# Performance work log

Measured on AMD Instinct MI355X. Metric: run time of the kernel, lower is better.

## Reference

```python
import jax, jax.numpy as jnp
import numpy as np

B, T, E, H, C = 64, 512, 768, 128, 18


def setup_inputs() -> dict:
    key = jax.random.key(0)
    ks = jax.random.split(key, 16)
    s = 1.0 / np.sqrt(H)
    inp = {
        "x": jax.random.normal(ks[0], (B, T, E), jnp.float32),
        "attention_mask": jnp.ones((B, T), jnp.int32),
        "labels": jax.random.randint(ks[1], (B, T), 0, C, jnp.int32),
        "Wih_f": jax.random.uniform(ks[2], (4 * H, E), jnp.float32, -s, s),
        "Whh_f": jax.random.uniform(ks[3], (4 * H, H), jnp.float32, -s, s),
        "b_f": jax.random.uniform(ks[4], (4 * H,), jnp.float32, -s, s),
        "Wih_b": jax.random.uniform(ks[5], (4 * H, E), jnp.float32, -s, s),
        "Whh_b": jax.random.uniform(ks[6], (4 * H, H), jnp.float32, -s, s),
        "b_b": jax.random.uniform(ks[7], (4 * H,), jnp.float32, -s, s),
        "Wfc": jax.random.uniform(ks[8], (C, 2 * H), jnp.float32, -s, s),
        "bfc": jax.random.uniform(ks[9], (C,), jnp.float32, -s, s),
        "start_trans": jax.random.normal(ks[10], (C,), jnp.float32) * 0.1,
        "end_trans": jax.random.normal(ks[11], (C,), jnp.float32) * 0.1,
        "trans": jax.random.normal(ks[12], (C, C), jnp.float32) * 0.1,
    }
    return inp


def _lstm_dir(x, Wih, Whh, b, reverse=False):
    # x: [B, T, E] -> hidden states [B, T, H]; torch LSTM gate order i,f,g,o
    if reverse:
        x = x[:, ::-1]
    pre = jnp.einsum("bte,ge->btg", x, Wih) + b  # [B, T, 4H] input projection once
    h0 = jnp.zeros((x.shape[0], H), x.dtype)

    def step(carry, pt):
        h, c = carry
        g = pt + h @ Whh.T
        i, f, gg, o = jnp.split(g, 4, axis=-1)
        c = jax.nn.sigmoid(f) * c + jax.nn.sigmoid(i) * jnp.tanh(gg)
        h = jax.nn.sigmoid(o) * jnp.tanh(c)
        return (h, c), h

    _, hs = jax.lax.scan(step, (h0, h0), jnp.swapaxes(pre, 0, 1))
    hs = jnp.swapaxes(hs, 0, 1)
    if reverse:
        hs = hs[:, ::-1]
    return hs


def _crf_loglik(em, tags, mask, start, end, trans):
    # pytorch-crf log-likelihood, batch_first. em [B,T,C], tags/mask [B,T]
    b, t, _ = em.shape
    maskf = mask.astype(em.dtype)
    tags = tags.astype(jnp.int32)
    # numerator: score of the given tag path
    em_sc = jnp.take_along_axis(em, tags[..., None], axis=2)[..., 0]  # [B,T]
    num = start[tags[:, 0]] + em_sc[:, 0]
    num = num + jnp.sum(em_sc[:, 1:] * maskf[:, 1:], axis=1)
    num = num + jnp.sum(trans[tags[:, :-1], tags[:, 1:]] * maskf[:, 1:], axis=1)
    last_idx = jnp.sum(mask.astype(jnp.int32), axis=1) - 1
    last_tags = jnp.take_along_axis(tags, last_idx[:, None], axis=1)[:, 0]
    num = num + end[last_tags]
    # denominator: forward algorithm (logsumexp recurrence over time)
    alpha0 = start + em[:, 0]  # [B,C]

    def step(alpha, inp):
        e_t, m_t = inp
        new = jax.scipy.special.logsumexp(alpha[:, :, None] + trans[None], axis=1) + e_t
        return jnp.where(m_t[:, None], new, alpha), None

    alpha, _ = jax.lax.scan(
        step, alpha0,
        (jnp.swapaxes(em[:, 1:], 0, 1), jnp.swapaxes(mask[:, 1:].astype(bool), 0, 1)),
    )
    den = jax.scipy.special.logsumexp(alpha + end, axis=1)
    return num - den


def _viterbi(em, start, end, trans):
    # em [B,T,C] -> best path [B,T] (full mask)
    s0 = start + em[:, 0]

    def fstep(score, e_t):
        cand = score[:, :, None] + trans[None]  # [B,C,C]
        return jnp.max(cand, axis=1) + e_t, jnp.argmax(cand, axis=1)

    score, bptr = jax.lax.scan(fstep, s0, jnp.swapaxes(em[:, 1:], 0, 1))  # bptr [T-1,B,C]
    last = jnp.argmax(score + end, axis=1)  # [B]

    def bstep(tag, ptr_t):
        prev = jnp.take_along_axis(ptr_t, tag[:, None], axis=1)[:, 0]
        return prev, prev

    _, path = jax.lax.scan(bstep, last, bptr, reverse=True)  # [T-1,B]
    return jnp.concatenate([jnp.swapaxes(path, 0, 1), last[:, None]], axis=1)


def reference(x, attention_mask, labels, Wih_f, Whh_f, b_f, Wih_b, Whh_b, b_b,
              Wfc, bfc, start_trans, end_trans, trans):
    hf = _lstm_dir(x, Wih_f, Whh_f, b_f, reverse=False)
    hb = _lstm_dir(x, Wih_b, Whh_b, b_b, reverse=True)
    seq = jnp.concatenate([hf, hb], axis=-1)  # [B,T,2H]
    em = seq @ Wfc.T + bfc  # [B,T,C] emissions
    mask = attention_mask.astype(bool)
    llh = _crf_loglik(em, labels, mask, start_trans, end_trans, trans)
    loss = -jnp.sum(llh) / x.shape[0]  # reduction='sum' then / batch_size
    path = _viterbi(em, start_trans, end_trans, trans) + 1  # res_paths = x+1
    return path, loss
```

## Files before the change

### kernel.cpp

```cpp
#include <hip/hip_runtime.h>
#include <hip/hip_bf16.h>
#include <math.h>

typedef __attribute__((ext_vector_type(8))) short short8;
typedef __attribute__((ext_vector_type(4))) float f32x4;

constexpr int nB = 64, nT = 512, nE = 768, nH = 128, nG = 512, nC = 18;
constexpr int nBT = nB * nT;

__device__ __forceinline__ float bf2f(unsigned short u) { return __uint_as_float(((unsigned int)u) << 16); }
__device__ __forceinline__ unsigned short f2bf(float f) {
  __hip_bfloat16 h = __float2bfloat16(f);
  return *reinterpret_cast<unsigned short*>(&h);
}
__device__ __forceinline__ float fast_sig(float x) {
  return __builtin_amdgcn_rcpf(1.0f + __builtin_amdgcn_exp2f(-1.44269504f * x));
}
__device__ __forceinline__ float fast_tanh(float x) {
  return 1.0f - 2.0f * __builtin_amdgcn_rcpf(1.0f + __builtin_amdgcn_exp2f(2.88539008f * x));
}
__device__ __forceinline__ float fast_exp(float x) { return __builtin_amdgcn_exp2f(1.44269504f * x); }
__device__ __forceinline__ float fast_log(float x) { return __builtin_amdgcn_logf(x) * 0.69314718f; }

__global__ __launch_bounds__(256) void cvt_kernel(const float* __restrict__ in,
                                                  unsigned short* __restrict__ out, int n8) {
  int i = blockIdx.x * blockDim.x + threadIdx.x;
  const int stride = gridDim.x * blockDim.x;
  for (; i < n8; i += stride) {
    const float4 a = ((const float4*)in)[(size_t)i * 2];
    const float4 b = ((const float4*)in)[(size_t)i * 2 + 1];
    unsigned short u[8] = {f2bf(a.x), f2bf(a.y), f2bf(a.z), f2bf(a.w),
                           f2bf(b.x), f2bf(b.y), f2bf(b.z), f2bf(b.w)};
    ((float4*)out)[i] = *(float4*)u;
  }
}

__global__ __launch_bounds__(256) void proj_kernel(
    const unsigned short* __restrict__ xbf,
    const unsigned short* __restrict__ wfb, const unsigned short* __restrict__ wbb,
    const float* __restrict__ biasF, const float* __restrict__ biasB,
    unsigned short* __restrict__ Pf, unsigned short* __restrict__ Pb)
{
  const int bid = blockIdx.x;
  const int mt = bid & 255, sub = bid >> 8;
  const int dir = sub >> 2, nt = sub & 3;
  const unsigned short* W = dir ? wbb : wfb;
  const float* bias = dir ? biasB : biasF;
  unsigned short* P = dir ? Pb : Pf;
  const int m0 = mt * 128, n0 = nt * 128;

  __shared__ unsigned short As[128 * 40];
  __shared__ unsigned short Bs[128 * 40];
  const int tid = threadIdx.x;
  const int w = tid >> 6, lane = tid & 63, l15 = lane & 15, l4 = lane >> 4;
  const int wr = w >> 1, wc = w & 1;
  const int srow = tid >> 1, shalf = tid & 1;

  const unsigned short* srcA = xbf + (size_t)(m0 + srow) * nE + shalf * 16;
  const unsigned short* srcB = W + (size_t)(n0 + srow) * nE + shalf * 16;

  f32x4 acc[4][4];
#pragma unroll
  for (int i = 0; i < 4; ++i)
#pragma unroll
    for (int j = 0; j < 4; ++j) acc[i][j] = (f32x4){0.f, 0.f, 0.f, 0.f};

  for (int k0 = 0; k0 < nE; k0 += 32) {
    const float4 a0 = *(const float4*)(srcA + k0);
    const float4 a1 = *(const float4*)(srcA + k0 + 8);
    const float4 b0 = *(const float4*)(srcB + k0);
    const float4 b1 = *(const float4*)(srcB + k0 + 8);
    __syncthreads();
    *(float4*)&As[srow * 40 + shalf * 16] = a0;
    *(float4*)&As[srow * 40 + shalf * 16 + 8] = a1;
    *(float4*)&Bs[srow * 40 + shalf * 16] = b0;
    *(float4*)&Bs[srow * 40 + shalf * 16 + 8] = b1;
    __syncthreads();
    short8 af[4], bfr[4];
#pragma unroll
    for (int i = 0; i < 4; ++i) af[i] = *(const short8*)&As[(wr * 64 + i * 16 + l15) * 40 + l4 * 8];
#pragma unroll
    for (int j = 0; j < 4; ++j) bfr[j] = *(const short8*)&Bs[(wc * 64 + j * 16 + l15) * 40 + l4 * 8];
#pragma unroll
    for (int i = 0; i < 4; ++i)
#pragma unroll
      for (int j = 0; j < 4; ++j)
        acc[i][j] = __builtin_amdgcn_mfma_f32_16x16x32_bf16(af[i], bfr[j], acc[i][j], 0, 0, 0);
  }
  float bv[4];
#pragma unroll
  for (int j = 0; j < 4; ++j) bv[j] = bias[n0 + wc * 64 + j * 16 + l15];
#pragma unroll
  for (int i = 0; i < 4; ++i) {
#pragma unroll
    for (int j = 0; j < 4; ++j) {
      const int col = n0 + wc * 64 + j * 16 + l15;
#pragma unroll
      for (int r = 0; r < 4; ++r) {
        const int row = m0 + wr * 64 + i * 16 + l4 * 4 + r;
        P[(size_t)row * nG + col] = f2bf(acc[i][j][r] + bv[j]);
      }
    }
  }
}

__global__ __launch_bounds__(512, 1) void lstm_kernel(
    const unsigned short* __restrict__ Pf, const unsigned short* __restrict__ Pb,
    const float* __restrict__ WhhF, const float* __restrict__ WhhB,
    unsigned short* __restrict__ hf, unsigned short* __restrict__ hb)
{
  const int bid = blockIdx.x;
  const int dir = bid & 1, grp = bid >> 1;
  const int b0 = grp * 4;
  const unsigned short* pre = dir ? Pb : Pf;
  const float* Whh = dir ? WhhB : WhhF;
  unsigned short* hout = dir ? hb : hf;

  const int tid = threadIdx.x, w = tid >> 6, lane = tid & 63;
  const int l15 = lane & 15, l4 = lane >> 4;
  const int batch = l15 & 3, msel = l15 >> 2;
  const int cell = w * 16 + msel * 4 + l4;
  const int swz = batch * 40;

  __shared__ unsigned short h_lds[2 * 4 * 128];

  short8 Af[4][4];
#pragma unroll
  for (int m = 0; m < 4; ++m) {
    const int gp = w * 64 + m * 16 + l15;
    const int gorig = (gp & 3) * 128 + (gp >> 2);
#pragma unroll
    for (int kk = 0; kk < 4; ++kk) {
      const float* wp = Whh + (size_t)gorig * nH + kk * 32 + l4 * 8;
      const float4 v0 = *(const float4*)wp;
      const float4 v1 = *(const float4*)(wp + 4);
      unsigned short u[8] = {f2bf(v0.x), f2bf(v0.y), f2bf(v0.z), f2bf(v0.w),
                             f2bf(v1.x), f2bf(v1.y), f2bf(v1.z), f2bf(v1.w)};
      Af[m][kk] = *(short8*)u;
    }
  }
  for (int i = tid; i < 2 * 4 * 128; i += 512) h_lds[i] = 0;

  float c_state = 0.f;
  const unsigned short* pbase = pre + (size_t)(b0 + batch) * nT * nG + cell;

  unsigned short pA[4], pB[4];
  {
    const int tt0 = dir ? (nT - 1) : 0;
    const int tt1 = dir ? (nT - 2) : 1;
#pragma unroll
    for (int r = 0; r < 4; ++r) pA[r] = pbase[(size_t)tt0 * nG + r * 128];
#pragma unroll
    for (int r = 0; r < 4; ++r) pB[r] = pbase[(size_t)tt1 * nG + r * 128];
  }
  __syncthreads();

#define LSTM_STEP(RB, T, BUFC)                                                   \
  {                                                                              \
    const int ttime = dir ? (nT - 1 - (T)) : (T);                                \
    float pg[4];                                                                 \
    _Pragma("unroll")                                                            \
    for (int r = 0; r < 4; ++r) pg[r] = bf2f(BUFC[r]);                           \
    {                                                                            \
      const int tl = ((T) + 2 < nT) ? (T) + 2 : (T);                             \
      const int ttl = dir ? (nT - 1 - tl) : tl;                                  \
      _Pragma("unroll")                                                          \
      for (int r = 0; r < 4; ++r) BUFC[r] = pbase[(size_t)ttl * nG + r * 128];   \
    }                                                                            \
    short8 bfr[4];                                                               \
    _Pragma("unroll")                                                            \
    for (int kk = 0; kk < 4; ++kk) {                                             \
      const int idx = (RB) * 512 + batch * 128 + ((kk * 32 + l4 * 8) ^ swz);     \
      bfr[kk] = *(const short8*)&h_lds[idx];                                     \
    }                                                                            \
    f32x4 acc[4];                                                                \
    _Pragma("unroll")                                                            \
    for (int m = 0; m < 4; ++m) acc[m] = (f32x4){0.f, 0.f, 0.f, 0.f};            \
    _Pragma("unroll")                                                            \
    for (int kk = 0; kk < 4; ++kk)                                               \
      _Pragma("unroll")                                                          \
      for (int m = 0; m < 4; ++m)                                                \
        acc[m] = __builtin_amdgcn_mfma_f32_16x16x32_bf16(Af[m][kk], bfr[kk], acc[m], 0, 0, 0); \
    const float g0 = msel < 2 ? (msel == 0 ? acc[0][0] : acc[1][0]) : (msel == 2 ? acc[2][0] : acc[3][0]); \
    const float g1 = msel < 2 ? (msel == 0 ? acc[0][1] : acc[1][1]) : (msel == 2 ? acc[2][1] : acc[3][1]); \
    const float g2 = msel < 2 ? (msel == 0 ? acc[0][2] : acc[1][2]) : (msel == 2 ? acc[2][2] : acc[3][2]); \
    const float g3 = msel < 2 ? (msel == 0 ? acc[0][3] : acc[1][3]) : (msel == 2 ? acc[2][3] : acc[3][3]); \
    const float gi = g0 + pg[0], gf = g1 + pg[1], gg = g2 + pg[2], go = g3 + pg[3]; \
    c_state = fast_sig(gf) * c_state + fast_sig(gi) * fast_tanh(gg);             \
    const float hval = fast_sig(go) * fast_tanh(c_state);                        \
    const unsigned short hu = f2bf(hval);                                        \
    h_lds[((RB) ^ 1) * 512 + batch * 128 + (cell ^ swz)] = hu;                   \
    hout[((size_t)(b0 + batch) * nT + ttime) * nH + cell] = hu;                  \
    asm volatile("s_waitcnt lgkmcnt(0)" ::: "memory");                           \
    __builtin_amdgcn_sched_barrier(0);                                           \
    __builtin_amdgcn_s_barrier();                                                \
  }

  for (int t2 = 0; t2 < nT; t2 += 2) {
    LSTM_STEP(0, t2, pA)
    LSTM_STEP(1, t2 + 1, pB)
  }
#undef LSTM_STEP
}

__global__ __launch_bounds__(256) void em_kernel(
    const unsigned short* __restrict__ hf, const unsigned short* __restrict__ hb,
    const float* __restrict__ Wfc, const float* __restrict__ bfc,
    float* __restrict__ em)
{
  __shared__ float seq[32][260];
  __shared__ float Wf[18][260];
  const int tid = threadIdx.x;
  const int row0 = blockIdx.x * 32;
  for (int i = tid; i < 32 * 32; i += 256) {
    const int r = i >> 5, seg = i & 31;
    const unsigned short* src = (seg < 16) ? (hf + (size_t)(row0 + r) * nH + seg * 8)
                                           : (hb + (size_t)(row0 + r) * nH + (seg - 16) * 8);
    const float4 v = *(const float4*)src;
    const unsigned short* u = (const unsigned short*)&v;
#pragma unroll
    for (int k = 0; k < 8; ++k) seq[r][seg * 8 + k] = bf2f(u[k]);
  }
  for (int i = tid; i < nC * 256; i += 256) {
    const int cc = i >> 8, k = i & 255;
    Wf[cc][k] = Wfc[cc * 256 + k];
  }
  __syncthreads();
  for (int o = tid; o < 32 * nC; o += 256) {
    const int r = o / nC, cc = o - r * nC;
    float acc = bfc[cc];
    const float4* s4 = (const float4*)&seq[r][0];
    const float4* w4 = (const float4*)&Wf[cc][0];
#pragma unroll
    for (int q = 0; q < 64; ++q) {
      const float4 a = s4[q]; const float4 wv = w4[q];
      acc += a.x * wv.x + a.y * wv.y + a.z * wv.z + a.w * wv.w;
    }
    em[(size_t)(row0 + r) * nC + cc] = acc;
  }
}

__global__ __launch_bounds__(128) void crfvit_kernel(
    const float* __restrict__ em, const int* __restrict__ labels,
    const int* __restrict__ mask, const float* __restrict__ start,
    const float* __restrict__ endt, const float* __restrict__ trans,
    float* __restrict__ llh, float* __restrict__ out_path)
{
  const int b = blockIdx.x; const int tid = threadIdx.x;
  __shared__ float tr[nC * nC];
  __shared__ float alpha[nC];
  __shared__ float score[nC];
  __shared__ unsigned char bp[(nT - 1) * nC];
  __shared__ unsigned char path[nT];
  for (int i = tid; i < nC * nC; i += 128) tr[i] = trans[i];
  __syncthreads();
  const float* eb = em + (size_t)b * nT * nC;

  if (tid < 64) {
    const int l = tid;
    const int* tg = labels + (size_t)b * nT;
    const int* mk = mask + (size_t)b * nT;
    float np = 0.f; int cnt = 0;
    for (int t = l; t < nT; t += 64) {
      const int tag = tg[t];
      const float e = eb[(size_t)t * nC + tag];
      if (t == 0) np += start[tag] + e;
      else np += (float)mk[t] * (e + tr[tg[t - 1] * nC + tag]);
      cnt += mk[t];
    }
#pragma unroll
    for (int off = 32; off; off >>= 1) { np += __shfl_xor(np, off); cnt += __shfl_xor(cnt, off); }
    float num = np + endt[tg[cnt - 1]];

    if (l < nC) alpha[l] = start[l] + eb[l];
    float epre = (l < nC) ? eb[nC + l] : 0.f;
    __builtin_amdgcn_wave_barrier();
    for (int t = 1; t < nT; ++t) {
      const float ecur = epre;
      if (l < nC && t + 1 < nT) epre = eb[(size_t)(t + 1) * nC + l];
      float anew = 0.f;
      if (l < nC) {
        const float aold = alpha[l];
        float cand[nC];
        float m = -3.0e38f;
#pragma unroll
        for (int i = 0; i < nC; ++i) { cand[i] = alpha[i] + tr[i * nC + l]; m = fmaxf(m, cand[i]); }
        float s = 0.f;
#pragma unroll
        for (int i = 0; i < nC; ++i) s += fast_exp(cand[i] - m);
        anew = m + fast_log(s) + ecur;
        if (mk[t] == 0) anew = aold;
      }
      __builtin_amdgcn_wave_barrier();
      if (l < nC) alpha[l] = anew;
      __builtin_amdgcn_wave_barrier();
    }
    const float v = (l < nC) ? (alpha[l] + endt[l]) : -3.0e38f;
    float m = v;
#pragma unroll
    for (int off = 32; off; off >>= 1) m = fmaxf(m, __shfl_xor(m, off));
    float s = (l < nC) ? fast_exp(v - m) : 0.f;
#pragma unroll
    for (int off = 32; off; off >>= 1) s += __shfl_xor(s, off);
    if (l == 0) llh[b] = num - (m + fast_log(s));
  } else {
    const int l = tid - 64;
    if (l < nC) score[l] = start[l] + eb[l];
    float epre = (l < nC) ? eb[nC + l] : 0.f;
    __builtin_amdgcn_wave_barrier();
    for (int t = 1; t < nT; ++t) {
      const float ecur = epre;
      if (l < nC && t + 1 < nT) epre = eb[(size_t)(t + 1) * nC + l];
      float m = -3.0e38f; int arg = 0;
      if (l < nC) {
#pragma unroll
        for (int i = 0; i < nC; ++i) {
          const float v = score[i] + tr[i * nC + l];
          if (v > m) { m = v; arg = i; }
        }
        m += ecur;
      }
      __builtin_amdgcn_wave_barrier();
      if (l < nC) { score[l] = m; bp[(t - 1) * nC + l] = (unsigned char)arg; }
      __builtin_amdgcn_wave_barrier();
    }
    if (l == 0) {
      float m = -3.0e38f; int last = 0;
      for (int i = 0; i < nC; ++i) { const float v = score[i] + endt[i]; if (v > m) { m = v; last = i; } }
      path[nT - 1] = (unsigned char)last;
      int cur = last;
      for (int t = nT - 2; t >= 0; --t) { cur = bp[t * nC + cur]; path[t] = (unsigned char)cur; }
    }
    __builtin_amdgcn_wave_barrier();
    __builtin_amdgcn_s_waitcnt(0);
    for (int t = l; t < nT; t += 64) out_path[(size_t)b * nT + t] = (float)(path[t] + 1);
  }
}

__global__ __launch_bounds__(64) void loss_kernel(const float* __restrict__ llh, float* __restrict__ out)
{
  const int l = threadIdx.x;
  float v = llh[l];
#pragma unroll
  for (int off = 32; off; off >>= 1) v += __shfl_xor(v, off);
  if (l == 0) out[0] = -v / (float)nB;
}

extern "C" void kernel_launch(void* const* d_in, const int* in_sizes, int n_in,
                              void* d_out, int out_size, void* d_ws, size_t ws_size,
                              hipStream_t stream)
{
  const float* x      = (const float*)d_in[0];
  const int*   amask  = (const int*)d_in[1];
  const int*   labels = (const int*)d_in[2];
  const float* Wih_f  = (const float*)d_in[3];
  const float* Whh_f  = (const float*)d_in[4];
  const float* b_f    = (const float*)d_in[5];
  const float* Wih_b  = (const float*)d_in[6];
  const float* Whh_b  = (const float*)d_in[7];
  const float* b_b    = (const float*)d_in[8];
  const float* Wfc    = (const float*)d_in[9];
  const float* bfc    = (const float*)d_in[10];
  const float* start  = (const float*)d_in[11];
  const float* endt   = (const float*)d_in[12];
  const float* trans  = (const float*)d_in[13];

  float* out = (float*)d_out;
  float* ws = (float*)d_ws;
  unsigned short* preF = (unsigned short*)ws;
  unsigned short* preB = preF + (size_t)nBT * nG;
  unsigned short* hf   = preB + (size_t)nBT * nG;
  unsigned short* hb   = hf + (size_t)nBT * nH;
  float* em  = (float*)(hb + (size_t)nBT * nH);
  float* llh = em + (size_t)nBT * nC;
  unsigned short* xbf = (unsigned short*)(llh + 64);
  unsigned short* wfb = xbf + (size_t)nBT * nE;
  unsigned short* wbb = wfb + (size_t)nG * nE;

  cvt_kernel<<<4096, 256, 0, stream>>>(x, xbf, nBT * nE / 8);
  cvt_kernel<<<192, 256, 0, stream>>>(Wih_f, wfb, nG * nE / 8);
  cvt_kernel<<<192, 256, 0, stream>>>(Wih_b, wbb, nG * nE / 8);
  proj_kernel<<<2048, 256, 0, stream>>>(xbf, wfb, wbb, b_f, b_b, preF, preB);
  lstm_kernel<<<32, 512, 0, stream>>>(preF, preB, Whh_f, Whh_b, hf, hb);
  em_kernel<<<1024, 256, 0, stream>>>(hf, hb, Wfc, bfc, em);
  crfvit_kernel<<<64, 128, 0, stream>>>(em, labels, amask, start, endt, trans, llh, out);
  loss_kernel<<<1, 64, 0, stream>>>(llh, out + nBT);
}
```

Baseline: 630.0 us.

## Fuse x bf16 conversion into projection GEMM; register-resident CRF/Viterbi recurrences

Drops the separate kernel that converts x to bf16. The projection GEMM now loads fp32 x directly and converts it while staging into shared memory, which removes a full write and re-read of the bf16 copy of x. The CRF forward and Viterbi loops now keep alpha and score in registers and broadcast them with readlane instead of shared memory, using a register-cached transition column, a tree max, mask ballots, and a three-step emission prefetch. In exchange, the GEMM reads twice as many bytes per A tile and repeats the conversion in each N-tile block (8x redundant), and the CRF loops use more registers.

```diff
diff --git a/kernel.cpp b/kernel.cpp
--- a/kernel.cpp
+++ b/kernel.cpp
@@ -12,6 +12,9 @@
 __device__ __forceinline__ unsigned short f2bf(float f) {
   __hip_bfloat16 h = __float2bfloat16(f);
   return *reinterpret_cast<unsigned short*>(&h);
+}
+__device__ __forceinline__ float rlane(float v, int lane) {
+  return __uint_as_float(__builtin_amdgcn_readlane(__float_as_uint(v), lane));
 }
 __device__ __forceinline__ float fast_sig(float x) {
   return __builtin_amdgcn_rcpf(1.0f + __builtin_amdgcn_exp2f(-1.44269504f * x));
@@ -36,7 +39,7 @@
 }
 
 __global__ __launch_bounds__(256) void proj_kernel(
-    const unsigned short* __restrict__ xbf,
+    const float* __restrict__ x,
     const unsigned short* __restrict__ wfb, const unsigned short* __restrict__ wbb,
     const float* __restrict__ biasF, const float* __restrict__ biasB,
     unsigned short* __restrict__ Pf, unsigned short* __restrict__ Pb)
@@ -56,7 +59,7 @@
   const int wr = w >> 1, wc = w & 1;
   const int srow = tid >> 1, shalf = tid & 1;
 
-  const unsigned short* srcA = xbf + (size_t)(m0 + srow) * nE + shalf * 16;
+  const float* srcA = x + (size_t)(m0 + srow) * nE + shalf * 16;
   const unsigned short* srcB = W + (size_t)(n0 + srow) * nE + shalf * 16;
 
   f32x4 acc[4][4];
@@ -67,12 +70,18 @@
 
   for (int k0 = 0; k0 < nE; k0 += 32) {
     const float4 a0 = *(const float4*)(srcA + k0);
-    const float4 a1 = *(const float4*)(srcA + k0 + 8);
+    const float4 a1 = *(const float4*)(srcA + k0 + 4);
+    const float4 a2 = *(const float4*)(srcA + k0 + 8);
+    const float4 a3 = *(const float4*)(srcA + k0 + 12);
     const float4 b0 = *(const float4*)(srcB + k0);
     const float4 b1 = *(const float4*)(srcB + k0 + 8);
+    unsigned short ua[16] = {f2bf(a0.x), f2bf(a0.y), f2bf(a0.z), f2bf(a0.w),
+                             f2bf(a1.x), f2bf(a1.y), f2bf(a1.z), f2bf(a1.w),
+                             f2bf(a2.x), f2bf(a2.y), f2bf(a2.z), f2bf(a2.w),
+                             f2bf(a3.x), f2bf(a3.y), f2bf(a3.z), f2bf(a3.w)};
     __syncthreads();
-    *(float4*)&As[srow * 40 + shalf * 16] = a0;
-    *(float4*)&As[srow * 40 + shalf * 16 + 8] = a1;
+    *(float4*)&As[srow * 40 + shalf * 16] = *(float4*)&ua[0];
+    *(float4*)&As[srow * 40 + shalf * 16 + 8] = *(float4*)&ua[8];
     *(float4*)&Bs[srow * 40 + shalf * 16] = b0;
     *(float4*)&Bs[srow * 40 + shalf * 16 + 8] = b1;
     __syncthreads();
@@ -248,18 +257,22 @@
 {
   const int b = blockIdx.x; const int tid = threadIdx.x;
   __shared__ float tr[nC * nC];
-  __shared__ float alpha[nC];
-  __shared__ float score[nC];
   __shared__ unsigned char bp[(nT - 1) * nC];
   __shared__ unsigned char path[nT];
   for (int i = tid; i < nC * nC; i += 128) tr[i] = trans[i];
   __syncthreads();
   const float* eb = em + (size_t)b * nT * nC;
 
+#define MAX18(c) fmaxf(fmaxf(fmaxf(fmaxf(fmaxf(c[0], c[1]), c[2]), fmaxf(fmaxf(c[3], c[4]), c[5])),           \
+                             fmaxf(fmaxf(fmaxf(c[6], c[7]), c[8]), fmaxf(fmaxf(c[9], c[10]), c[11]))),        \
+                       fmaxf(fmaxf(fmaxf(c[12], c[13]), c[14]), fmaxf(fmaxf(c[15], c[16]), c[17])))
+
   if (tid < 64) {
     const int l = tid;
+    const int lc = l < nC ? l : nC - 1;
     const int* tg = labels + (size_t)b * nT;
     const int* mk = mask + (size_t)b * nT;
+
     float np = 0.f; int cnt = 0;
     for (int t = l; t < nT; t += 64) {
       const int tag = tg[t];
@@ -270,32 +283,38 @@
     }
 #pragma unroll
     for (int off = 32; off; off >>= 1) { np += __shfl_xor(np, off); cnt += __shfl_xor(cnt, off); }
-    float num = np + endt[tg[cnt - 1]];
-
-    if (l < nC) alpha[l] = start[l] + eb[l];
-    float epre = (l < nC) ? eb[nC + l] : 0.f;
-    __builtin_amdgcn_wave_barrier();
-    for (int t = 1; t < nT; ++t) {
-      const float ecur = epre;
-      if (l < nC && t + 1 < nT) epre = eb[(size_t)(t + 1) * nC + l];
-      float anew = 0.f;
-      if (l < nC) {
-        const float aold = alpha[l];
+    const float num = np + endt[tg[cnt - 1]];
+
+    float trc[nC];
+#pragma unroll
+    for (int i = 0; i < nC; ++i) trc[i] = tr[i * nC + lc];
+
+    float alpha_r = start[lc] + eb[lc];
+    float eA = eb[1 * nC + lc];
+    float eB = eb[2 * nC + lc];
+    float eC = eb[3 * nC + lc];
+    for (int tk = 0; tk < 8; ++tk) {
+      const unsigned long long mb = __ballot(mk[tk * 64 + l] != 0);
+      for (int tt = (tk == 0 ? 1 : 0); tt < 64; ++tt) {
+        const int t = tk * 64 + tt;
+        const float ecur = eA; eA = eB; eB = eC;
+        const int tl = t + 3 < nT ? t + 3 : nT - 1;
+        eC = eb[(size_t)tl * nC + lc];
         float cand[nC];
-        float m = -3.0e38f;
-#pragma unroll
-        for (int i = 0; i < nC; ++i) { cand[i] = alpha[i] + tr[i * nC + l]; m = fmaxf(m, cand[i]); }
+#pragma unroll
+        for (int i = 0; i < nC; ++i) cand[i] = rlane(alpha_r, i) + trc[i];
+        const float m = MAX18(cand);
+        float ex[nC];
+#pragma unroll
+        for (int i = 0; i < nC; ++i) ex[i] = fast_exp(cand[i] - m);
         float s = 0.f;
 #pragma unroll
-        for (int i = 0; i < nC; ++i) s += fast_exp(cand[i] - m);
-        anew = m + fast_log(s) + ecur;
-        if (mk[t] == 0) anew = aold;
+        for (int i = 0; i < nC; ++i) s += ex[i];
+        const float anew = m + fast_log(s) + ecur;
+        alpha_r = ((mb >> tt) & 1) ? anew : alpha_r;
       }
-      __builtin_amdgcn_wave_barrier();
-      if (l < nC) alpha[l] = anew;
-      __builtin_amdgcn_wave_barrier();
-    }
-    const float v = (l < nC) ? (alpha[l] + endt[l]) : -3.0e38f;
+    }
+    const float v = (l < nC) ? (alpha_r + endt[l]) : -3.0e38f;
     float m = v;
 #pragma unroll
     for (int off = 32; off; off >>= 1) m = fmaxf(m, __shfl_xor(m, off));
@@ -305,36 +324,47 @@
     if (l == 0) llh[b] = num - (m + fast_log(s));
   } else {
     const int l = tid - 64;
-    if (l < nC) score[l] = start[l] + eb[l];
-    float epre = (l < nC) ? eb[nC + l] : 0.f;
-    __builtin_amdgcn_wave_barrier();
+    const int lc = l < nC ? l : nC - 1;
+    float trc[nC];
+#pragma unroll
+    for (int i = 0; i < nC; ++i) trc[i] = tr[i * nC + lc];
+
+    float score_r = start[lc] + eb[lc];
+    float eA = eb[1 * nC + lc];
+    float eB = eb[2 * nC + lc];
+    float eC = eb[3 * nC + lc];
     for (int t = 1; t < nT; ++t) {
-      const float ecur = epre;
-      if (l < nC && t + 1 < nT) epre = eb[(size_t)(t + 1) * nC + l];
-      float m = -3.0e38f; int arg = 0;
-      if (l < nC) {
-#pragma unroll
-        for (int i = 0; i < nC; ++i) {
-          const float v = score[i] + tr[i * nC + l];
-          if (v > m) { m = v; arg = i; }
-        }
-        m += ecur;
+      const float ecur = eA; eA = eB; eB = eC;
+      const int tl = t + 3 < nT ? t + 3 : nT - 1;
+      eC = eb[(size_t)tl * nC + lc];
+      float cand[nC];
+#pragma unroll
+      for (int i = 0; i < nC; ++i) cand[i] = rlane(score_r, i) + trc[i];
+      const float m = MAX18(cand);
+      int sel[nC];
+#pragma unroll
+      for (int i = 0; i < nC; ++i) sel[i] = (cand[i] == m) ? i : 63;
+      int arg = sel[0];
+#pragma unroll
+      for (int i = 1; i < nC; ++i) arg = min(arg, sel[i]);
+      score_r = m + ecur;
+      if (l < nC) bp[(t - 1) * nC + l] = (unsigned char)arg;
+    }
+    if (l == 0) {
+      float mm = -3.0e38f; int last = 0;
+      for (int i = 0; i < nC; ++i) {
+        const float v = rlane(score_r, i) + endt[i];
+        if (v > mm) { mm = v; last = i; }
       }
-      __builtin_amdgcn_wave_barrier();
-      if (l < nC) { score[l] = m; bp[(t - 1) * nC + l] = (unsigned char)arg; }
-      __builtin_amdgcn_wave_barrier();
-    }
-    if (l == 0) {
-      float m = -3.0e38f; int last = 0;
-      for (int i = 0; i < nC; ++i) { const float v = score[i] + endt[i]; if (v > m) { m = v; last = i; } }
       path[nT - 1] = (unsigned char)last;
       int cur = last;
       for (int t = nT - 2; t >= 0; --t) { cur = bp[t * nC + cur]; path[t] = (unsigned char)cur; }
     }
+    asm volatile("s_waitcnt lgkmcnt(0)" ::: "memory");
     __builtin_amdgcn_wave_barrier();
-    __builtin_amdgcn_s_waitcnt(0);
     for (int t = l; t < nT; t += 64) out_path[(size_t)b * nT + t] = (float)(path[t] + 1);
   }
+#undef MAX18
 }
 
 __global__ __launch_bounds__(64) void loss_kernel(const float* __restrict__ llh, float* __restrict__ out)
@@ -373,14 +403,12 @@
   unsigned short* hb   = hf + (size_t)nBT * nH;
   float* em  = (float*)(hb + (size_t)nBT * nH);
   float* llh = em + (size_t)nBT * nC;
-  unsigned short* xbf = (unsigned short*)(llh + 64);
-  unsigned short* wfb = xbf + (size_t)nBT * nE;
+  unsigned short* wfb = (unsigned short*)(llh + 64);
   unsigned short* wbb = wfb + (size_t)nG * nE;
 
-  cvt_kernel<<<4096, 256, 0, stream>>>(x, xbf, nBT * nE / 8);
   cvt_kernel<<<192, 256, 0, stream>>>(Wih_f, wfb, nG * nE / 8);
   cvt_kernel<<<192, 256, 0, stream>>>(Wih_b, wbb, nG * nE / 8);
-  proj_kernel<<<2048, 256, 0, stream>>>(xbf, wfb, wbb, b_f, b_b, preF, preB);
+  proj_kernel<<<2048, 256, 0, stream>>>(x, wfb, wbb, b_f, b_b, preF, preB);
   lstm_kernel<<<32, 512, 0, stream>>>(preF, preB, Whh_f, Whh_b, hf, hb);
   em_kernel<<<1024, 256, 0, stream>>>(hf, hb, Wfc, bfc, em);
   crfvit_kernel<<<64, 128, 0, stream>>>(em, labels, amask, start, endt, trans, llh, out);
```

Result: faster. 549.0 us (-12.9%).
